# Kernel tuning notes

Measured on AMD Instinct MI355X. Metric: run time of the kernel, lower is better.

## Reference

```python
import jax, jax.numpy as jnp
import numpy as np

N = 4096      # number of nodes (seq_len); > 1000 so dag positional encoding is skipped
IN = 45       # input_dim
HID = 256     # hidden_dim
NH = 4        # num_heads
DH = HID // NH
E = 131072    # edges (avg degree 32)
# bucketed time bias: (lo, hi, weight)
BUCKETS = ((0.0, 5.0, 0.2), (5.0, 15.0, 0.1), (15.0, 60.0, 0.0), (60.0, 240.0, -0.1))
NEG = -1e9


def setup_inputs() -> dict:
    key = jax.random.key(0)
    ks = jax.random.split(key, 16)

    def lin_w(k, fan_in, fan_out):
        return (jax.random.normal(k, (fan_in, fan_out), jnp.float32) / np.float32(np.sqrt(fan_in)))

    return {
        "node_features": jax.random.normal(ks[0], (N, IN), jnp.float32),
        "temporal_data": jax.random.uniform(ks[1], (N, N, 2), jnp.float32) * 300.0,  # dt minutes in [0,300)
        "edge_index": jax.random.randint(ks[2], (2, E), 0, N),
        "W_in": lin_w(ks[3], IN, HID), "b_in": jnp.zeros((HID,), jnp.float32),
        "Wq": lin_w(ks[4], HID, HID), "bq": jnp.zeros((HID,), jnp.float32),
        "Wk": lin_w(ks[5], HID, HID), "bk": jnp.zeros((HID,), jnp.float32),
        "Wv": lin_w(ks[6], HID, HID), "bv": jnp.zeros((HID,), jnp.float32),
        "Wo": lin_w(ks[7], HID, HID), "bo": jnp.zeros((HID,), jnp.float32),
    }


def reference(node_features, temporal_data, edge_index, W_in, b_in, Wq, bq, Wk, bk, Wv, bv, Wo, bo):
    L = node_features.shape[0]
    x = node_features @ W_in + b_in                      # [L, HID]; pos-enc skipped since L > 1000

    def heads(W, b):
        return (x @ W + b).reshape(L, NH, DH).transpose(1, 0, 2)  # [NH, L, DH]

    q, k, v = heads(Wq, bq), heads(Wk, bk), heads(Wv, bv)

    scores = jnp.einsum('hld,hsd->hls', q, k) / np.float32(np.sqrt(DH))  # [NH, L, L]

    # bucketed time bias from dt_minutes
    dt = temporal_data[:, :, 0]
    tb = jnp.zeros_like(dt)
    for lo, hi, w in BUCKETS:
        tb = tb + np.float32(w) * ((dt >= lo) & (dt <= hi)).astype(dt.dtype)
    scores = scores + tb[None]                           # broadcast over heads

    # edge mask: True blocks attention; edges and self-loops allowed
    u, vdst = edge_index[0], edge_index[1]
    block = jnp.ones((L, L), dtype=bool).at[u, vdst].set(False)
    diag = jnp.arange(L)
    block = block.at[diag, diag].set(False)
    scores = jnp.where(block[None], NEG, scores)

    attn = jax.nn.softmax(scores, axis=-1)               # eval mode: no dropout
    out = jnp.einsum('hls,hsd->hld', attn, v)            # [NH, L, DH]
    out = out.transpose(1, 0, 2).reshape(L, HID)         # [L, HID]
    return out @ Wo + bo
```

## Files before the change

kernel.cpp:

```cpp
#include <hip/hip_runtime.h>
#include <hip/hip_bf16.h>
#include <stdint.h>

#define N_NODES 4096
#define HIDDEN 256
#define NHEAD 4
#define DHEAD 64
#define NEDGE 131072
#define MASK_WORDS 128
#define KIN 64
#define MAXDEG 1024

typedef __attribute__((ext_vector_type(8))) short bf16x8;
typedef __attribute__((ext_vector_type(4))) float f32x4;
typedef __hip_bfloat16 bf16;

__device__ __forceinline__ float b2f(short s) {
    union { float f; unsigned u; } x;
    x.u = ((unsigned)(unsigned short)s) << 16;
    return x.f;
}

__global__ __launch_bounds__(256) void prep_kernel(
    const int* __restrict__ eidx, const float* __restrict__ nf,
    const float* __restrict__ W_in, const float* __restrict__ b_in,
    const float* __restrict__ Wq, const float* __restrict__ bq,
    const float* __restrict__ Wk, const float* __restrict__ bk,
    const float* __restrict__ Wv, const float* __restrict__ bv,
    const float* __restrict__ Wo,
    unsigned int* __restrict__ mask, bf16* __restrict__ nfp,
    bf16* __restrict__ WqkvT, float* __restrict__ bqkv,
    bf16* __restrict__ WoT)
{
    int t = blockIdx.x * 256 + threadIdx.x;
    if (t < NEDGE) {
        int u = eidx[t], v = eidx[NEDGE + t];
        atomicOr(&mask[u * MASK_WORDS + (v >> 5)], 1u << (v & 31));
        return;
    }
    t -= NEDGE;
    if (t < N_NODES) {
        atomicOr(&mask[t * MASK_WORDS + (t >> 5)], 1u << (t & 31));
        return;
    }
    t -= N_NODES;
    if (t < N_NODES * KIN) {
        int row = t >> 6, c = t & 63;
        float v = (c < 45) ? nf[row * 45 + c] : 0.f;
        nfp[t] = __float2bfloat16(v);
        return;
    }
    t -= N_NODES * KIN;
    if (t < 3 * 256 * KIN) {
        int which = t >> 14, r = t & 16383;
        int n = r & 255, kk = r >> 8;
        const float* W = (which == 0) ? Wq : (which == 1) ? Wk : Wv;
        float dot = 0.f;
        if (kk < 45) {
            const float* wrow = W_in + kk * 256;
            for (int c = 0; c < 256; ++c)
                dot += wrow[c] * W[c * 256 + n];
        }
        WqkvT[(size_t)which * 16384 + (size_t)n * KIN + kk] = __float2bfloat16(dot);
        return;
    }
    t -= 3 * 256 * KIN;
    if (t < 3 * 256) {
        int which = t >> 8, n = t & 255;
        const float* W = (which == 0) ? Wq : (which == 1) ? Wk : Wv;
        const float* b = (which == 0) ? bq : (which == 1) ? bk : bv;
        float acc = b[n];
        for (int c = 0; c < 256; ++c)
            acc += b_in[c] * W[c * 256 + n];
        bqkv[t] = acc;
        return;
    }
    t -= 3 * 256;
    if (t < 65536) {
        int kk = t >> 8, n = t & 255;
        WoT[(size_t)n * 256 + kk] = __float2bfloat16(Wo[(size_t)kk * 256 + n]);
    }
}

template <bool OUT_BF16>
__device__ __forceinline__ void gemm_body(
    const bf16* __restrict__ A, const bf16* __restrict__ Bt,
    const float* __restrict__ bias, void* __restrict__ Cv,
    int K, int m_base, int n0)
{
    const int lane = threadIdx.x & 63;
    const int row = lane & 15, quad = lane >> 4;
    f32x4 acc0 = {0.f, 0.f, 0.f, 0.f};
    f32x4 acc1 = {0.f, 0.f, 0.f, 0.f};
    const short* Ap = (const short*)A;
    const short* Bp = (const short*)Bt;

    for (int k0 = 0; k0 < K; k0 += 32) {
        bf16x8 b  = *(const bf16x8*)(Bp + (size_t)(n0 + row) * K + k0 + quad * 8);
        bf16x8 a0 = *(const bf16x8*)(Ap + (size_t)(m_base + row) * K + k0 + quad * 8);
        bf16x8 a1 = *(const bf16x8*)(Ap + (size_t)(m_base + 16 + row) * K + k0 + quad * 8);
        acc0 = __builtin_amdgcn_mfma_f32_16x16x32_bf16(a0, b, acc0, 0, 0, 0);
        acc1 = __builtin_amdgcn_mfma_f32_16x16x32_bf16(a1, b, acc1, 0, 0, 0);
    }

    const int col = row;
    const float bval = bias[n0 + col];
#pragma unroll
    for (int e = 0; e < 4; ++e) {
        int m0 = m_base + quad * 4 + e;
        int m1 = m0 + 16;
        float v0 = acc0[e] + bval;
        float v1 = acc1[e] + bval;
        if (OUT_BF16) {
            ((bf16*)Cv)[(size_t)m0 * HIDDEN + n0 + col] = __float2bfloat16(v0);
            ((bf16*)Cv)[(size_t)m1 * HIDDEN + n0 + col] = __float2bfloat16(v1);
        } else {
            ((float*)Cv)[(size_t)m0 * HIDDEN + n0 + col] = v0;
            ((float*)Cv)[(size_t)m1 * HIDDEN + n0 + col] = v1;
        }
    }
}

__global__ __launch_bounds__(256) void gemm_qkv_kernel(
    const bf16* __restrict__ nfp, const bf16* __restrict__ WqkvT,
    const float* __restrict__ bqkv,
    float* __restrict__ q, bf16* __restrict__ k, bf16* __restrict__ v)
{
    int which = blockIdx.x >> 4;
    const bf16* Bt = WqkvT + (size_t)which * 16384;
    const float* bias = bqkv + which * 256;
    int wave = threadIdx.x >> 6;
    int mb = blockIdx.y * 128 + wave * 32;
    int n0 = (blockIdx.x & 15) * 16;
    if (which == 0)      gemm_body<false>(nfp, Bt, bias, q, KIN, mb, n0);
    else if (which == 1) gemm_body<true>(nfp, Bt, bias, k, KIN, mb, n0);
    else                 gemm_body<true>(nfp, Bt, bias, v, KIN, mb, n0);
}

__global__ __launch_bounds__(256) void gemm_out_kernel(
    const bf16* __restrict__ att, const bf16* __restrict__ WoT,
    const float* __restrict__ bo, float* __restrict__ out)
{
    int wave = threadIdx.x >> 6;
    gemm_body<false>(att, WoT, bo, out, HIDDEN,
                     blockIdx.y * 128 + wave * 32, blockIdx.x * 16);
}

__global__ __launch_bounds__(256) void attn_kernel(
    const float* __restrict__ q, const bf16* __restrict__ k,
    const bf16* __restrict__ v, const float* __restrict__ temporal,
    const unsigned int* __restrict__ mask, bf16* __restrict__ att)
{
    __shared__ int jlist[MAXDEG];
    __shared__ float qs[HIDDEN];
    __shared__ float pj[NHEAD][64];
    __shared__ int cnt;
    const int i = blockIdx.x, tid = threadIdx.x;

    if (tid == 0) cnt = 0;
    qs[tid] = q[(size_t)i * HIDDEN + tid];
    __syncthreads();
    if (tid < MASK_WORDS) {
        unsigned int bits = mask[(size_t)i * MASK_WORDS + tid];
        int n = __popc(bits);
        if (n) {
            int pos = atomicAdd(&cnt, n);
            while (bits) {
                int b = __ffs(bits) - 1;
                bits &= bits - 1;
                if (pos < MAXDEG) jlist[pos] = (tid << 5) + b;
                ++pos;
            }
        }
    }
    __syncthreads();
    const int nn = cnt;

    const int h = tid >> 6, lane = tid & 63;
    const float* trow = temporal + (size_t)i * N_NODES * 2;
    const short* kp = (const short*)k;
    const short* vp = (const short*)v;
    const float* qh = qs + h * DHEAD;

    float l = 0.f, acc = 0.f;

    for (int c0 = 0; c0 < nn; c0 += 64) {
        const int cend = min(64, nn - c0);
        float s = -3.0e38f;
        if (lane < cend) {
            int j = jlist[c0 + lane];
            float dt = trow[(size_t)j * 2];
            const short* krow = kp + (size_t)j * HIDDEN + h * DHEAD;
            bf16x8 k8[8];
#pragma unroll
            for (int t = 0; t < 8; ++t)
                k8[t] = *(const bf16x8*)(krow + t * 8);
            float dot = 0.f;
#pragma unroll
            for (int t = 0; t < 8; ++t)
#pragma unroll
                for (int e = 0; e < 8; ++e)
                    dot += b2f(k8[t][e]) * qh[t * 8 + e];
            float tb = 0.f;
            tb += 0.2f * (float)((dt >= 0.f)  & (dt <= 5.f));
            tb += 0.1f * (float)((dt >= 5.f)  & (dt <= 15.f));
            tb -= 0.1f * (float)((dt >= 60.f) & (dt <= 240.f));
            s = dot * 0.125f + tb;
        }
        float p = __expf(s);
        float csum = p;
#pragma unroll
        for (int off = 32; off >= 1; off >>= 1)
            csum += __shfl_xor(csum, off, 64);
        pj[h][lane] = p;
        l += csum;
        for (int u = 0; u < cend; u += 8) {
#pragma unroll
            for (int t = 0; t < 8; ++t) {
                int idx = u + t;
                bool valid = idx < cend;
                int j = jlist[c0 + (valid ? idx : 0)];
                float pv = valid ? pj[h][idx] : 0.f;
                float vf = b2f(vp[(size_t)j * HIDDEN + h * DHEAD + lane]);
                acc += pv * vf;
            }
        }
    }

    att[(size_t)i * HIDDEN + h * DHEAD + lane] = __float2bfloat16(acc / l);
}

extern "C" void kernel_launch(void* const* d_in, const int* in_sizes, int n_in,
                              void* d_out, int out_size, void* d_ws, size_t ws_size,
                              hipStream_t stream) {
    const float* nf       = (const float*)d_in[0];
    const float* temporal = (const float*)d_in[1];
    const int*   eidx     = (const int*)  d_in[2];
    const float* W_in     = (const float*)d_in[3];
    const float* b_in     = (const float*)d_in[4];
    const float* Wq       = (const float*)d_in[5];
    const float* bq       = (const float*)d_in[6];
    const float* Wk       = (const float*)d_in[7];
    const float* bk       = (const float*)d_in[8];
    const float* Wv       = (const float*)d_in[9];
    const float* bv       = (const float*)d_in[10];
    const float* Wo       = (const float*)d_in[11];
    const float* bo       = (const float*)d_in[12];
    float* out = (float*)d_out;

    char* ws = (char*)d_ws;
    const size_t MiB = 1 << 20, KiB = 1 << 10;
    unsigned int* mask = (unsigned int*)(ws);
    bf16*  nfp   = (bf16*)(ws + 2 * MiB);
    bf16*  WqkvT = (bf16*)(ws + 2 * MiB + 512 * KiB);
    float* bqkv  = (float*)(ws + 2 * MiB + 640 * KiB);
    bf16*  WoT   = (bf16*)(ws + 3 * MiB);
    float* q     = (float*)(ws + 4 * MiB);
    bf16*  kb    = (bf16*)(ws + 8 * MiB);
    bf16*  vb    = (bf16*)(ws + 10 * MiB);
    bf16*  att   = (bf16*)(ws + 12 * MiB);

    hipMemsetAsync(mask, 0, (size_t)N_NODES * MASK_WORDS * sizeof(unsigned int), stream);

    {
        int total = NEDGE + N_NODES + N_NODES * KIN + 3 * 256 * KIN + 3 * 256 + 65536;
        prep_kernel<<<(total + 255) / 256, 256, 0, stream>>>(
            eidx, nf, W_in, b_in, Wq, bq, Wk, bk, Wv, bv, Wo,
            mask, nfp, WqkvT, bqkv, WoT);
    }

    gemm_qkv_kernel<<<dim3(48, 32), 256, 0, stream>>>(nfp, WqkvT, bqkv, q, kb, vb);

    attn_kernel<<<N_NODES, 256, 0, stream>>>(q, kb, vb, temporal, mask, att);

    gemm_out_kernel<<<dim3(16, 32), 256, 0, stream>>>(att, WoT, bo, out);
}
```

Measured before the change: 250.9 us.

## Fold mask clearing into prep, fuse edge scatter with QKV GEMM, vectorize V gather

The separate memset is removed and the mask is zeroed inside the prep kernel. The edge-bit scatter moves from prep into the QKV GEMM launch as extra blocks, so the scatter and the GEMM run concurrently in one grid. In attention, each lane now loads a pair of bf16 V values and the two half-waves handle alternating neighbours, combined with a shuffle at the end. This removes one launch and halves the V gather instruction count, at the cost of an extra cross-half reduction.

```diff
diff --git a/kernel.cpp b/kernel.cpp
--- a/kernel.cpp
+++ b/kernel.cpp
@@ -15,14 +15,18 @@
 typedef __attribute__((ext_vector_type(4))) float f32x4;
 typedef __hip_bfloat16 bf16;
 
-__device__ __forceinline__ float b2f(short s) {
+__device__ __forceinline__ float b2f(unsigned short s) {
     union { float f; unsigned u; } x;
-    x.u = ((unsigned)(unsigned short)s) << 16;
+    x.u = ((unsigned)s) << 16;
     return x.f;
 }
+__device__ __forceinline__ unsigned short f2bu(float f) {
+    bf16 b = __float2bfloat16(f);
+    return *(unsigned short*)&b;
+}
 
 __global__ __launch_bounds__(256) void prep_kernel(
-    const int* __restrict__ eidx, const float* __restrict__ nf,
+    const float* __restrict__ nf,
     const float* __restrict__ W_in, const float* __restrict__ b_in,
     const float* __restrict__ Wq, const float* __restrict__ bq,
     const float* __restrict__ Wk, const float* __restrict__ bk,
@@ -33,17 +37,11 @@
     bf16* __restrict__ WoT)
 {
     int t = blockIdx.x * 256 + threadIdx.x;
-    if (t < NEDGE) {
-        int u = eidx[t], v = eidx[NEDGE + t];
-        atomicOr(&mask[u * MASK_WORDS + (v >> 5)], 1u << (v & 31));
-        return;
-    }
-    t -= NEDGE;
-    if (t < N_NODES) {
-        atomicOr(&mask[t * MASK_WORDS + (t >> 5)], 1u << (t & 31));
-        return;
-    }
-    t -= N_NODES;
+    if (t < 131072) {
+        ((uint4*)mask)[t] = make_uint4(0, 0, 0, 0);
+        return;
+    }
+    t -= 131072;
     if (t < N_NODES * KIN) {
         int row = t >> 6, c = t & 63;
         float v = (c < 45) ? nf[row * 45 + c] : 0.f;
@@ -121,29 +119,35 @@
     }
 }
 
-__global__ __launch_bounds__(256) void gemm_qkv_kernel(
+__global__ __launch_bounds__(256) void qkv_scatter_kernel(
     const bf16* __restrict__ nfp, const bf16* __restrict__ WqkvT,
-    const float* __restrict__ bqkv,
-    float* __restrict__ q, bf16* __restrict__ k, bf16* __restrict__ v)
-{
-    int which = blockIdx.x >> 4;
-    const bf16* Bt = WqkvT + (size_t)which * 16384;
-    const float* bias = bqkv + which * 256;
-    int wave = threadIdx.x >> 6;
-    int mb = blockIdx.y * 128 + wave * 32;
-    int n0 = (blockIdx.x & 15) * 16;
-    if (which == 0)      gemm_body<false>(nfp, Bt, bias, q, KIN, mb, n0);
-    else if (which == 1) gemm_body<true>(nfp, Bt, bias, k, KIN, mb, n0);
-    else                 gemm_body<true>(nfp, Bt, bias, v, KIN, mb, n0);
-}
-
-__global__ __launch_bounds__(256) void gemm_out_kernel(
-    const bf16* __restrict__ att, const bf16* __restrict__ WoT,
-    const float* __restrict__ bo, float* __restrict__ out)
-{
-    int wave = threadIdx.x >> 6;
-    gemm_body<false>(att, WoT, bo, out, HIDDEN,
-                     blockIdx.y * 128 + wave * 32, blockIdx.x * 16);
+    const float* __restrict__ bqkv, const int* __restrict__ eidx,
+    float* __restrict__ q, bf16* __restrict__ k, bf16* __restrict__ v,
+    unsigned int* __restrict__ mask)
+{
+    int bx = blockIdx.x;
+    if (bx < 1536) {
+        int ntile = bx >> 5, mrow = bx & 31;
+        int which = ntile >> 4;
+        const bf16* Bt = WqkvT + (size_t)which * 16384;
+        const float* bias = bqkv + which * 256;
+        int wave = threadIdx.x >> 6;
+        int mb = mrow * 128 + wave * 32;
+        int n0 = (ntile & 15) * 16;
+        if (which == 0)      gemm_body<false>(nfp, Bt, bias, q, KIN, mb, n0);
+        else if (which == 1) gemm_body<true>(nfp, Bt, bias, k, KIN, mb, n0);
+        else                 gemm_body<true>(nfp, Bt, bias, v, KIN, mb, n0);
+        return;
+    }
+    int t = (bx - 1536) * 256 + threadIdx.x;
+    if (t < NEDGE) {
+        int u = eidx[t], w = eidx[NEDGE + t];
+        atomicOr(&mask[u * MASK_WORDS + (w >> 5)], 1u << (w & 31));
+    } else {
+        int i = t - NEDGE;
+        if (i < N_NODES)
+            atomicOr(&mask[i * MASK_WORDS + (i >> 5)], 1u << (i & 31));
+    }
 }
 
 __global__ __launch_bounds__(256) void attn_kernel(
@@ -177,12 +181,13 @@
     const int nn = cnt;
 
     const int h = tid >> 6, lane = tid & 63;
+    const int half = lane >> 5, dpair = lane & 31;
     const float* trow = temporal + (size_t)i * N_NODES * 2;
-    const short* kp = (const short*)k;
-    const short* vp = (const short*)v;
+    const unsigned short* kp = (const unsigned short*)k;
+    const unsigned short* vp = (const unsigned short*)v;
     const float* qh = qs + h * DHEAD;
 
-    float l = 0.f, acc = 0.f;
+    float l = 0.f, acc0 = 0.f, acc1 = 0.f;
 
     for (int c0 = 0; c0 < nn; c0 += 64) {
         const int cend = min(64, nn - c0);
@@ -190,7 +195,7 @@
         if (lane < cend) {
             int j = jlist[c0 + lane];
             float dt = trow[(size_t)j * 2];
-            const short* krow = kp + (size_t)j * HIDDEN + h * DHEAD;
+            const unsigned short* krow = kp + (size_t)j * HIDDEN + h * DHEAD;
             bf16x8 k8[8];
 #pragma unroll
             for (int t = 0; t < 8; ++t)
@@ -200,7 +205,7 @@
             for (int t = 0; t < 8; ++t)
 #pragma unroll
                 for (int e = 0; e < 8; ++e)
-                    dot += b2f(k8[t][e]) * qh[t * 8 + e];
+                    dot += b2f((unsigned short)k8[t][e]) * qh[t * 8 + e];
             float tb = 0.f;
             tb += 0.2f * (float)((dt >= 0.f)  & (dt <= 5.f));
             tb += 0.1f * (float)((dt >= 5.f)  & (dt <= 15.f));
@@ -214,20 +219,38 @@
             csum += __shfl_xor(csum, off, 64);
         pj[h][lane] = p;
         l += csum;
-        for (int u = 0; u < cend; u += 8) {
-#pragma unroll
-            for (int t = 0; t < 8; ++t) {
-                int idx = u + t;
+        for (int u0 = 0; u0 < cend; u0 += 8) {
+#pragma unroll
+            for (int t = 0; t < 4; ++t) {
+                int idx = u0 + 2 * t + half;
                 bool valid = idx < cend;
                 int j = jlist[c0 + (valid ? idx : 0)];
                 float pv = valid ? pj[h][idx] : 0.f;
-                float vf = b2f(vp[(size_t)j * HIDDEN + h * DHEAD + lane]);
-                acc += pv * vf;
+                const unsigned short* vrow = vp + (size_t)j * HIDDEN + h * DHEAD + dpair * 2;
+                ushort2 v2 = *(const ushort2*)vrow;
+                acc0 += pv * b2f(v2.x);
+                acc1 += pv * b2f(v2.y);
             }
         }
     }
 
-    att[(size_t)i * HIDDEN + h * DHEAD + lane] = __float2bfloat16(acc / l);
+    acc0 += __shfl_xor(acc0, 32, 64);
+    acc1 += __shfl_xor(acc1, 32, 64);
+    if (half == 0) {
+        ushort2 o;
+        o.x = f2bu(acc0 / l);
+        o.y = f2bu(acc1 / l);
+        *(ushort2*)((unsigned short*)att + (size_t)i * HIDDEN + h * DHEAD + dpair * 2) = o;
+    }
+}
+
+__global__ __launch_bounds__(256) void gemm_out_kernel(
+    const bf16* __restrict__ att, const bf16* __restrict__ WoT,
+    const float* __restrict__ bo, float* __restrict__ out)
+{
+    int wave = threadIdx.x >> 6;
+    gemm_body<false>(att, WoT, bo, out, HIDDEN,
+                     blockIdx.y * 128 + wave * 32, blockIdx.x * 16);
 }
 
 extern "C" void kernel_launch(void* const* d_in, const int* in_sizes, int n_in,
@@ -260,16 +283,15 @@
     bf16*  vb    = (bf16*)(ws + 10 * MiB);
     bf16*  att   = (bf16*)(ws + 12 * MiB);
 
-    hipMemsetAsync(mask, 0, (size_t)N_NODES * MASK_WORDS * sizeof(unsigned int), stream);
-
     {
-        int total = NEDGE + N_NODES + N_NODES * KIN + 3 * 256 * KIN + 3 * 256 + 65536;
+        int total = 131072 + N_NODES * KIN + 3 * 256 * KIN + 3 * 256 + 65536;
         prep_kernel<<<(total + 255) / 256, 256, 0, stream>>>(
-            eidx, nf, W_in, b_in, Wq, bq, Wk, bk, Wv, bv, Wo,
+            nf, W_in, b_in, Wq, bq, Wk, bk, Wv, bv, Wo,
             mask, nfp, WqkvT, bqkv, WoT);
     }
 
-    gemm_qkv_kernel<<<dim3(48, 32), 256, 0, stream>>>(nfp, WqkvT, bqkv, q, kb, vb);
+    qkv_scatter_kernel<<<1536 + 528, 256, 0, stream>>>(
+        nfp, WqkvT, bqkv, eidx, q, kb, vb, mask);
 
     attn_kernel<<<N_NODES, 256, 0, stream>>>(q, kb, vb, temporal, mask, att);
 
```

Result: no change. 247.2 us (-1.5%).
